# Kernel tuning notes

Measured on AMD Instinct MI355X. Metric: run time of the kernel, lower is better.

## Reference

```python
import jax, jax.numpy as jnp
import numpy as np

BETA = 0.25  # commitment cost

def setup_inputs() -> dict:
    key = jax.random.key(0)
    k1, k2 = jax.random.split(key)
    L, D, N = 65536, 64, 1024  # tokens, e_dim, n_e
    z = jax.random.normal(k1, (L, D), dtype=jnp.float32)
    scale = 1.0 / N  # matches nn.Embedding uniform_(-1/n_e, 1/n_e) with embed_init_scale=1.0
    embedding = jax.random.uniform(k2, (N, D), minval=-scale, maxval=scale, dtype=jnp.float32)
    return {"z": z, "embedding": embedding}

def reference(z, embedding):
    # Euclidean distance: ||z||^2 + ||e||^2 - 2 z.e  -> [L, N]
    d = (jnp.sum(z * z, axis=1, keepdims=True)
         + jnp.sum(embedding * embedding, axis=1)
         - 2.0 * z @ embedding.T)
    # get_index with topk=1, no gumbel: argmax(-d) == argmin(d)
    min_encoding_indices = jnp.argmin(d, axis=1)  # [L]
    # one-hot @ embedding == gather (get_embed_type='matmul')
    z_q = jnp.take(embedding, min_encoding_indices, axis=0)  # [L, D]
    # VQ loss: beta*||sg[z_q]-z||^2 + ||z_q-sg[z]||^2 (means)
    loss = (BETA * jnp.mean((jax.lax.stop_gradient(z_q) - z) ** 2)
            + jnp.mean((z_q - jax.lax.stop_gradient(z)) ** 2))
    # straight-through estimator
    z_q_st = z + jax.lax.stop_gradient(z_q - z)
    return z_q_st, loss, min_encoding_indices
```

## Files before the change

### kernel.cpp

```cpp
#include <hip/hip_runtime.h>
#include <float.h>

#define L_TOK 65536
#define DIM   64
#define NCODE 1024
#define KCAP  16

typedef __attribute__((ext_vector_type(8))) short bf16x8;
typedef __attribute__((ext_vector_type(4))) float f32x4;

__device__ __forceinline__ unsigned short f2bf(float f) {
    unsigned u = __float_as_uint(f);
    u += 0x7FFF + ((u >> 16) & 1);
    return (unsigned short)(u >> 16);
}
__device__ __forceinline__ unsigned f2ord(float f) {
    unsigned u = __float_as_uint(f);
    return (u & 0x80000000u) ? ~u : (u | 0x80000000u);
}
__device__ __forceinline__ float ord2f(unsigned o) {
    unsigned u = (o & 0x80000000u) ? (o & 0x7FFFFFFFu) : ~o;
    return __uint_as_float(u);
}

__global__ __launch_bounds__(256) void init_kernel(unsigned long long* __restrict__ key,
                                                   unsigned* __restrict__ thr_ord) {
    int i = blockIdx.x * 256 + threadIdx.x;
    key[i]     = ~0ull;
    thr_ord[i] = ~0u;
}

__global__ __launch_bounds__(256) void esum_kernel(const float* __restrict__ emb,
                                                   float* __restrict__ esum,
                                                   unsigned short* __restrict__ eb) {
    int n = blockIdx.x * 256 + threadIdx.x;
    if (n >= NCODE) return;
    const float* e = emb + ((size_t)n << 6);
    float s = 0.f;
#pragma unroll
    for (int k = 0; k < DIM; ++k) s = fmaf(e[k], e[k], s);
    esum[n] = s;
#pragma unroll
    for (int k = 0; k < DIM; ++k) eb[(n << 6) + k] = f2bf(e[k]);
}

__global__ __launch_bounds__(256) void prep_kernel(const float* __restrict__ z,
                                                   float* __restrict__ zs_out,
                                                   float* __restrict__ marg_out) {
    __shared__ float zl[256][65];
    const int t  = threadIdx.x;
    const int bb = blockIdx.x * 256;
    for (int i = t; i < 4096; i += 256) {
        float4 v = ((const float4*)(z + ((size_t)bb << 6)))[i];
        int tok = i >> 4, k = (i & 15) * 4;
        zl[tok][k] = v.x; zl[tok][k+1] = v.y; zl[tok][k+2] = v.z; zl[tok][k+3] = v.w;
    }
    __syncthreads();
    float zs = 0.f, sa = 0.f;
#pragma unroll
    for (int k = 0; k < DIM; ++k) {
        float v = zl[t][k];
        zs = fmaf(v, v, zs);
        sa += fabsf(v);
    }
    zs_out[bb + t]   = zs;
    marg_out[bb + t] = fmaf(sa, 2.4e-5f, 6e-5f);
}

__global__ __launch_bounds__(512, 2) void screen1_kernel(const float* __restrict__ z,
                                                         const unsigned short* __restrict__ eb,
                                                         const float* __restrict__ esum,
                                                         unsigned* __restrict__ thr_ord) {
    __shared__ unsigned short zbf[128 * 64];
    __shared__ float minw[8][128];

    const int t    = threadIdx.x;
    const int lane = t & 63;
    const int w    = __builtin_amdgcn_readfirstlane(t >> 6);
    const int bb   = (blockIdx.x >> 1) * 128;
    const int ch   = blockIdx.x & 1;
    char* zb = (char*)zbf;

    {
        const int row = t >> 2, q = t & 3;
        const int sw  = (row & 7) << 4;
        const float* zr = z + ((size_t)(bb + row) << 6) + q * 16;
        bf16x8 c0, c1;
#pragma unroll
        for (int i = 0; i < 8; ++i) { c0[i] = (short)f2bf(zr[i]); c1[i] = (short)f2bf(zr[i + 8]); }
        *(bf16x8*)(zb + row * 128 + ((q * 32) ^ sw))      = c0;
        *(bf16x8*)(zb + row * 128 + ((q * 32 + 16) ^ sw)) = c1;
    }

    const int r16 = lane & 15;
    const int kg  = lane >> 4;

    bf16x8 bq[4][2];
    float  esv[4];
#pragma unroll
    for (int ct = 0; ct < 4; ++ct) {
        const int code = ch * 512 + w * 64 + ct * 16 + r16;
        bq[ct][0] = *(const bf16x8*)(eb + ((size_t)code << 6) + kg * 8);
        bq[ct][1] = *(const bf16x8*)(eb + ((size_t)code << 6) + 32 + kg * 8);
        esv[ct]   = esum[code];
    }
    __syncthreads();

#pragma unroll
    for (int tile = 0; tile < 8; ++tile) {
        const int arow = tile * 16 + r16;
        const int asw  = (arow & 7) << 4;
        bf16x8 af0 = *(const bf16x8*)(zb + arow * 128 + ((kg * 16) ^ asw));
        bf16x8 af1 = *(const bf16x8*)(zb + arow * 128 + ((64 + kg * 16) ^ asw));
        f32x4 mnq = {FLT_MAX, FLT_MAX, FLT_MAX, FLT_MAX};
#pragma unroll
        for (int ct = 0; ct < 4; ++ct) {
            f32x4 acc = {0.f, 0.f, 0.f, 0.f};
            acc = __builtin_amdgcn_mfma_f32_16x16x32_bf16(af0, bq[ct][0], acc, 0, 0, 0);
            acc = __builtin_amdgcn_mfma_f32_16x16x32_bf16(af1, bq[ct][1], acc, 0, 0, 0);
#pragma unroll
            for (int r = 0; r < 4; ++r) {
                float q = fmaf(acc[r], -2.0f, esv[ct]);
                mnq[r] = fminf(mnq[r], q);
            }
        }
#pragma unroll
        for (int r = 0; r < 4; ++r) {
            float v = mnq[r];
            v = fminf(v, __shfl_xor(v, 1));
            v = fminf(v, __shfl_xor(v, 2));
            v = fminf(v, __shfl_xor(v, 4));
            v = fminf(v, __shfl_xor(v, 8));
            if (r16 == 0) minw[w][tile * 16 + kg * 4 + r] = v;
        }
    }
    __syncthreads();
    if (t < 128) {
        float m = minw[0][t];
#pragma unroll
        for (int ww = 1; ww < 8; ++ww) m = fminf(m, minw[ww][t]);
        atomicMin(&thr_ord[bb + t], f2ord(m));
    }
}

__global__ __launch_bounds__(512, 2) void screen2r_kernel(const float* __restrict__ z,
                                                          const unsigned short* __restrict__ eb,
                                                          const float* __restrict__ esum,
                                                          const float* __restrict__ zs_g,
                                                          const float* __restrict__ marg,
                                                          const unsigned* __restrict__ thr_ord,
                                                          const float* __restrict__ emb,
                                                          unsigned long long* __restrict__ key) {
    __shared__ unsigned short zbf[128 * 64];
    __shared__ float thr_l[128];
    __shared__ int   cnt_l[128];
    __shared__ unsigned short cand_l[128 * KCAP];
    __shared__ unsigned long long bestk[4][128];

    const int t    = threadIdx.x;
    const int lane = t & 63;
    const int w    = __builtin_amdgcn_readfirstlane(t >> 6);
    const int bb   = (blockIdx.x >> 1) * 128;
    const int ch   = blockIdx.x & 1;
    char* zb = (char*)zbf;

    {
        const int row = t >> 2, q = t & 3;
        const int sw  = (row & 7) << 4;
        const float* zr = z + ((size_t)(bb + row) << 6) + q * 16;
        bf16x8 c0, c1;
#pragma unroll
        for (int i = 0; i < 8; ++i) { c0[i] = (short)f2bf(zr[i]); c1[i] = (short)f2bf(zr[i + 8]); }
        *(bf16x8*)(zb + row * 128 + ((q * 32) ^ sw))      = c0;
        *(bf16x8*)(zb + row * 128 + ((q * 32 + 16) ^ sw)) = c1;
    }
    if (t < 128) {
        thr_l[t] = ord2f(thr_ord[bb + t]) + marg[bb + t];
        cnt_l[t] = 0;
    }

    const int r16 = lane & 15;
    const int kg  = lane >> 4;

    bf16x8 bq[4][2];
    float  esv[4];
#pragma unroll
    for (int ct = 0; ct < 4; ++ct) {
        const int code = ch * 512 + w * 64 + ct * 16 + r16;
        bq[ct][0] = *(const bf16x8*)(eb + ((size_t)code << 6) + kg * 8);
        bq[ct][1] = *(const bf16x8*)(eb + ((size_t)code << 6) + 32 + kg * 8);
        esv[ct]   = esum[code];
    }
    __syncthreads();

#pragma unroll
    for (int tile = 0; tile < 8; ++tile) {
        const int arow = tile * 16 + r16;
        const int asw  = (arow & 7) << 4;
        bf16x8 af0 = *(const bf16x8*)(zb + arow * 128 + ((kg * 16) ^ asw));
        bf16x8 af1 = *(const bf16x8*)(zb + arow * 128 + ((64 + kg * 16) ^ asw));
        float thrv[4];
#pragma unroll
        for (int r = 0; r < 4; ++r) thrv[r] = thr_l[tile * 16 + kg * 4 + r];
#pragma unroll
        for (int ct = 0; ct < 4; ++ct) {
            f32x4 acc = {0.f, 0.f, 0.f, 0.f};
            acc = __builtin_amdgcn_mfma_f32_16x16x32_bf16(af0, bq[ct][0], acc, 0, 0, 0);
            acc = __builtin_amdgcn_mfma_f32_16x16x32_bf16(af1, bq[ct][1], acc, 0, 0, 0);
#pragma unroll
            for (int r = 0; r < 4; ++r) {
                float q = fmaf(acc[r], -2.0f, esv[ct]);
                unsigned long long mask = __ballot(q <= thrv[r]);
                if (r16 == 0) {
                    unsigned bits = (unsigned)((mask >> (kg * 16)) & 0xFFFFull);
                    int tok = tile * 16 + kg * 4 + r;
                    while (bits) {
                        int b = __builtin_ctz(bits);
                        bits &= bits - 1;
                        int pos = atomicAdd(&cnt_l[tok], 1);
                        if (pos < KCAP)
                            cand_l[tok * KCAP + pos] =
                                (unsigned short)(ch * 512 + w * 64 + ct * 16 + b);
                    }
                }
            }
        }
    }
    __syncthreads();

    {
        const int tok   = t & 127;
        const int slot  = t >> 7;
        const int token = bb + tok;
        const float* zr = z + ((size_t)token << 6);
        const float  zsx = zs_g[token];
        const int    n   = cnt_l[tok];

        unsigned long long best = ~0ull;
        if (n <= KCAP) {
            for (int j = slot; j < n; j += 4) {
                int c = cand_l[tok * KCAP + j];
                const float* er = emb + ((size_t)c << 6);
                float a = 0.f;
#pragma unroll
                for (int k = 0; k < DIM; ++k) a = fmaf(zr[k], er[k], a);
                float d = fmaf(a, -2.0f, zsx + esum[c]);
                unsigned long long kk = ((unsigned long long)f2ord(d) << 32) | (unsigned)c;
                if (kk < best) best = kk;
            }
        } else {
            for (int c = ch * 512 + slot; c < ch * 512 + 512; c += 4) {
                const float* er = emb + ((size_t)c << 6);
                float a = 0.f;
#pragma unroll
                for (int k = 0; k < DIM; ++k) a = fmaf(zr[k], er[k], a);
                float d = fmaf(a, -2.0f, zsx + esum[c]);
                unsigned long long kk = ((unsigned long long)f2ord(d) << 32) | (unsigned)c;
                if (kk < best) best = kk;
            }
        }
        bestk[slot][tok] = best;
    }
    __syncthreads();
    if (t < 128) {
        unsigned long long b = bestk[0][t];
        if (bestk[1][t] < b) b = bestk[1][t];
        if (bestk[2][t] < b) b = bestk[2][t];
        if (bestk[3][t] < b) b = bestk[3][t];
        if (b != ~0ull) atomicMin(&key[bb + t], b);
    }
}

__global__ __launch_bounds__(256) void output_kernel(const float* __restrict__ z,
                                                     const float* __restrict__ emb,
                                                     const unsigned long long* __restrict__ key,
                                                     float* __restrict__ idx_out,
                                                     float* __restrict__ zq_out,
                                                     double* __restrict__ partials) {
    int gid = blockIdx.x * 256 + threadIdx.x;
    int l = gid >> 6;
    int k = gid & 63;
    int idx = (int)(unsigned)(key[l] & 0xFFFFFFFFull);

    float zv = z[gid];
    float ev = emb[(idx << 6) + k];
    float t    = ev - zv;
    float outv = zv + t;
    zq_out[gid] = outv;
    if (k == 0) idx_out[l] = (float)idx;

    float sq = t * t;

    __shared__ double red[256];
    red[threadIdx.x] = (double)sq;
    __syncthreads();
    for (int s = 128; s > 0; s >>= 1) {
        if (threadIdx.x < s) red[threadIdx.x] += red[threadIdx.x + s];
        __syncthreads();
    }
    if (threadIdx.x == 0) partials[blockIdx.x] = red[0];
}

__global__ __launch_bounds__(256) void loss_kernel(const double* __restrict__ partials,
                                                   float* __restrict__ loss_out) {
    __shared__ double red[256];
    int t = threadIdx.x;
    double s = 0.0;
    for (int i = 0; i < 64; ++i) s += partials[t * 64 + i];
    red[t] = s;
    __syncthreads();
    for (int st = 128; st > 0; st >>= 1) {
        if (t < st) red[t] += red[t + st];
        __syncthreads();
    }
    if (t == 0) {
        double m  = red[0] / (double)(L_TOK * DIM);
        float  mf = (float)m;
        loss_out[0] = 0.25f * mf + mf;
    }
}

extern "C" void kernel_launch(void* const* d_in, const int* in_sizes, int n_in,
                              void* d_out, int out_size, void* d_ws, size_t ws_size,
                              hipStream_t stream) {
    const float* z   = (const float*)d_in[0];
    const float* emb = (const float*)d_in[1];

    float* out   = (float*)d_out;
    float* zq    = out;
    float* loss  = out + 4194304;
    float* idxf  = out + 4194305;

    char* ws = (char*)d_ws;
    float*              esum     = (float*)ws;
    unsigned short*     eb       = (unsigned short*)(ws + 8192);
    float*              zs       = (float*)(ws + 139264);
    float*              marg     = (float*)(ws + 401408);
    double*             partials = (double*)(ws + 663552);
    unsigned long long* key      = (unsigned long long*)(ws + 794624);
    unsigned*           thr_ord  = (unsigned*)(ws + 1318912);

    init_kernel    <<<256,   256, 0, stream>>>(key, thr_ord);
    esum_kernel    <<<4,     256, 0, stream>>>(emb, esum, eb);
    prep_kernel    <<<256,   256, 0, stream>>>(z, zs, marg);
    screen1_kernel <<<1024,  512, 0, stream>>>(z, eb, esum, thr_ord);
    screen2r_kernel<<<1024,  512, 0, stream>>>(z, eb, esum, zs, marg, thr_ord, emb, key);
    output_kernel  <<<16384, 256, 0, stream>>>(z, emb, key, idxf, zq, partials);
    loss_kernel    <<<1,     256, 0, stream>>>(partials, loss);
}
```

Before: 98.69 us.

## Shrink screening pass to a 256-code subset, vectorize output, widen candidate cap

The first screening pass now checks only the first 256 codes, not all 1024, so each block covers 128 tokens with one write and needs no atomics or threshold init. That threshold is looser, so the per-token candidate capacity doubles to admit more survivors into the exact second pass. The output kernel moves to float4 loads and stores with wavefront shuffle reductions and fewer blocks, and the loss kernel is adjusted to match. A looser threshold may push more candidates into the second pass or overflow the cap, which could cost time or correctness.

```diff
diff --git a/kernel.cpp b/kernel.cpp
--- a/kernel.cpp
+++ b/kernel.cpp
@@ -4,7 +4,7 @@
 #define L_TOK 65536
 #define DIM   64
 #define NCODE 1024
-#define KCAP  16
+#define KCAP  32
 
 typedef __attribute__((ext_vector_type(8))) short bf16x8;
 typedef __attribute__((ext_vector_type(4))) float f32x4;
@@ -18,16 +18,10 @@
     unsigned u = __float_as_uint(f);
     return (u & 0x80000000u) ? ~u : (u | 0x80000000u);
 }
-__device__ __forceinline__ float ord2f(unsigned o) {
-    unsigned u = (o & 0x80000000u) ? (o & 0x7FFFFFFFu) : ~o;
-    return __uint_as_float(u);
-}
-
-__global__ __launch_bounds__(256) void init_kernel(unsigned long long* __restrict__ key,
-                                                   unsigned* __restrict__ thr_ord) {
+
+__global__ __launch_bounds__(256) void init_kernel(unsigned long long* __restrict__ key) {
     int i = blockIdx.x * 256 + threadIdx.x;
-    key[i]     = ~0ull;
-    thr_ord[i] = ~0u;
+    key[i] = ~0ull;
 }
 
 __global__ __launch_bounds__(256) void esum_kernel(const float* __restrict__ emb,
@@ -70,15 +64,14 @@
 __global__ __launch_bounds__(512, 2) void screen1_kernel(const float* __restrict__ z,
                                                          const unsigned short* __restrict__ eb,
                                                          const float* __restrict__ esum,
-                                                         unsigned* __restrict__ thr_ord) {
+                                                         float* __restrict__ thr_min) {
     __shared__ unsigned short zbf[128 * 64];
     __shared__ float minw[8][128];
 
     const int t    = threadIdx.x;
     const int lane = t & 63;
     const int w    = __builtin_amdgcn_readfirstlane(t >> 6);
-    const int bb   = (blockIdx.x >> 1) * 128;
-    const int ch   = blockIdx.x & 1;
+    const int bb   = blockIdx.x * 128;
     char* zb = (char*)zbf;
 
     {
@@ -95,11 +88,11 @@
     const int r16 = lane & 15;
     const int kg  = lane >> 4;
 
-    bf16x8 bq[4][2];
-    float  esv[4];
-#pragma unroll
-    for (int ct = 0; ct < 4; ++ct) {
-        const int code = ch * 512 + w * 64 + ct * 16 + r16;
+    bf16x8 bq[2][2];
+    float  esv[2];
+#pragma unroll
+    for (int ct = 0; ct < 2; ++ct) {
+        const int code = w * 32 + ct * 16 + r16;
         bq[ct][0] = *(const bf16x8*)(eb + ((size_t)code << 6) + kg * 8);
         bq[ct][1] = *(const bf16x8*)(eb + ((size_t)code << 6) + 32 + kg * 8);
         esv[ct]   = esum[code];
@@ -114,7 +107,7 @@
         bf16x8 af1 = *(const bf16x8*)(zb + arow * 128 + ((64 + kg * 16) ^ asw));
         f32x4 mnq = {FLT_MAX, FLT_MAX, FLT_MAX, FLT_MAX};
 #pragma unroll
-        for (int ct = 0; ct < 4; ++ct) {
+        for (int ct = 0; ct < 2; ++ct) {
             f32x4 acc = {0.f, 0.f, 0.f, 0.f};
             acc = __builtin_amdgcn_mfma_f32_16x16x32_bf16(af0, bq[ct][0], acc, 0, 0, 0);
             acc = __builtin_amdgcn_mfma_f32_16x16x32_bf16(af1, bq[ct][1], acc, 0, 0, 0);
@@ -139,7 +132,7 @@
         float m = minw[0][t];
 #pragma unroll
         for (int ww = 1; ww < 8; ++ww) m = fminf(m, minw[ww][t]);
-        atomicMin(&thr_ord[bb + t], f2ord(m));
+        thr_min[bb + t] = m;
     }
 }
 
@@ -148,7 +141,7 @@
                                                           const float* __restrict__ esum,
                                                           const float* __restrict__ zs_g,
                                                           const float* __restrict__ marg,
-                                                          const unsigned* __restrict__ thr_ord,
+                                                          const float* __restrict__ thr_min,
                                                           const float* __restrict__ emb,
                                                           unsigned long long* __restrict__ key) {
     __shared__ unsigned short zbf[128 * 64];
@@ -175,7 +168,7 @@
         *(bf16x8*)(zb + row * 128 + ((q * 32 + 16) ^ sw)) = c1;
     }
     if (t < 128) {
-        thr_l[t] = ord2f(thr_ord[bb + t]) + marg[bb + t];
+        thr_l[t] = thr_min[bb + t] + marg[bb + t];
         cnt_l[t] = 0;
     }
 
@@ -277,28 +270,32 @@
                                                      float* __restrict__ idx_out,
                                                      float* __restrict__ zq_out,
                                                      double* __restrict__ partials) {
-    int gid = blockIdx.x * 256 + threadIdx.x;
-    int l = gid >> 6;
-    int k = gid & 63;
-    int idx = (int)(unsigned)(key[l] & 0xFFFFFFFFull);
-
-    float zv = z[gid];
-    float ev = emb[(idx << 6) + k];
-    float t    = ev - zv;
-    float outv = zv + t;
-    zq_out[gid] = outv;
-    if (k == 0) idx_out[l] = (float)idx;
-
-    float sq = t * t;
-
-    __shared__ double red[256];
-    red[threadIdx.x] = (double)sq;
-    __syncthreads();
-    for (int s = 128; s > 0; s >>= 1) {
-        if (threadIdx.x < s) red[threadIdx.x] += red[threadIdx.x + s];
-        __syncthreads();
-    }
-    if (threadIdx.x == 0) partials[blockIdx.x] = red[0];
+    __shared__ double wsum[4];
+    const int gid  = blockIdx.x * 256 + threadIdx.x;
+    const int base = gid * 4;
+    const int l    = base >> 6;
+    const int k0   = base & 63;
+    const int idx  = (int)(unsigned)(key[l] & 0xFFFFFFFFull);
+
+    float4 zv = *(const float4*)(z + base);
+    float4 ev = *(const float4*)(emb + (idx << 6) + k0);
+    float tx = ev.x - zv.x, ty = ev.y - zv.y, tz = ev.z - zv.z, tw = ev.w - zv.w;
+    float4 o;
+    o.x = zv.x + tx; o.y = zv.y + ty; o.z = zv.z + tz; o.w = zv.w + tw;
+    *(float4*)(zq_out + base) = o;
+    if (k0 == 0) idx_out[l] = (float)idx;
+
+    double s = (double)(tx * tx);
+    s += (double)(ty * ty);
+    s += (double)(tz * tz);
+    s += (double)(tw * tw);
+
+#pragma unroll
+    for (int off = 32; off > 0; off >>= 1) s += __shfl_down(s, off);
+    if ((threadIdx.x & 63) == 0) wsum[threadIdx.x >> 6] = s;
+    __syncthreads();
+    if (threadIdx.x == 0)
+        partials[blockIdx.x] = wsum[0] + wsum[1] + wsum[2] + wsum[3];
 }
 
 __global__ __launch_bounds__(256) void loss_kernel(const double* __restrict__ partials,
@@ -306,7 +303,7 @@
     __shared__ double red[256];
     int t = threadIdx.x;
     double s = 0.0;
-    for (int i = 0; i < 64; ++i) s += partials[t * 64 + i];
+    for (int i = 0; i < 16; ++i) s += partials[t * 16 + i];
     red[t] = s;
     __syncthreads();
     for (int st = 128; st > 0; st >>= 1) {
@@ -337,14 +334,14 @@
     float*              zs       = (float*)(ws + 139264);
     float*              marg     = (float*)(ws + 401408);
     double*             partials = (double*)(ws + 663552);
-    unsigned long long* key      = (unsigned long long*)(ws + 794624);
-    unsigned*           thr_ord  = (unsigned*)(ws + 1318912);
-
-    init_kernel    <<<256,   256, 0, stream>>>(key, thr_ord);
-    esum_kernel    <<<4,     256, 0, stream>>>(emb, esum, eb);
-    prep_kernel    <<<256,   256, 0, stream>>>(z, zs, marg);
-    screen1_kernel <<<1024,  512, 0, stream>>>(z, eb, esum, thr_ord);
-    screen2r_kernel<<<1024,  512, 0, stream>>>(z, eb, esum, zs, marg, thr_ord, emb, key);
-    output_kernel  <<<16384, 256, 0, stream>>>(z, emb, key, idxf, zq, partials);
-    loss_kernel    <<<1,     256, 0, stream>>>(partials, loss);
-}
+    unsigned long long* key      = (unsigned long long*)(ws + 696320);
+    float*              thr_min  = (float*)(ws + 1220608);
+
+    init_kernel    <<<256,  256, 0, stream>>>(key);
+    esum_kernel    <<<4,    256, 0, stream>>>(emb, esum, eb);
+    prep_kernel    <<<256,  256, 0, stream>>>(z, zs, marg);
+    screen1_kernel <<<512,  512, 0, stream>>>(z, eb, esum, thr_min);
+    screen2r_kernel<<<1024, 512, 0, stream>>>(z, eb, esum, zs, marg, thr_min, emb, key);
+    output_kernel  <<<4096, 256, 0, stream>>>(z, emb, key, idxf, zq, partials);
+    loss_kernel    <<<1,    256, 0, stream>>>(partials, loss);
+}
```

Result: slower. 174.6 us (+76.9%).
